# Kernel tuning notes

Measured on AMD Instinct MI355X. Metric: run time of the kernel, lower is better.

## Reference

```python
import jax, jax.numpy as jnp
import numpy as np

# SOM hyperparameters (match init_kwargs)
M, N = 64, 64
NODES = M * N
FEATS = 256
BATCH = 1024
LR = 0.5
RADIUS_FACTOR = 1.1
TOTAL_ITER = 100000
SIGMA = max(M, N) * RADIUS_FACTOR


def setup_inputs() -> dict:
    key = jax.random.key(0)
    k1, k2 = jax.random.split(key)
    x = jax.random.uniform(k1, (BATCH, FEATS), dtype=jnp.float32)
    map_w = jax.random.uniform(k2, (NODES, FEATS), dtype=jnp.float32)
    return {"x": x, "map_w": map_w, "iteration": 0}


def _grid_locs():
    ii, jj = jnp.meshgrid(jnp.arange(M), jnp.arange(N), indexing='ij')
    return jnp.stack([ii.ravel(), jj.ravel()], axis=1)  # (NODES, 2) int32


def reference(x, map_w, iteration):
    B = x.shape[0]
    # ---- feedforward: squared distances (B, NODES) via GEMM expansion,
    # avoiding the (B, NODES, FEATS) broadcast the TF code materializes.
    x2 = jnp.sum(x * x, axis=1, keepdims=True)          # (B, 1)
    w2 = jnp.sum(map_w * map_w, axis=1)                  # (NODES,)
    sqd = x2 + w2[None, :] - 2.0 * (x @ map_w.T)         # (B, NODES)
    bmu_indices = jnp.argmin(sqd, axis=1)                # (B,)

    # ---- backprop: neighborhood-weighted codebook update
    locs = _grid_locs()                                  # (NODES, 2)
    bmu_locs = locs[bmu_indices]                         # (B, 2)
    # grid distance^2 between every node and each sample's BMU: (B, NODES)
    d2 = jnp.sum((locs[None, :, :] - bmu_locs[:, None, :]) ** 2, axis=2).astype(jnp.float32)

    lambda_g = TOTAL_ITER / SIGMA
    decay = jnp.exp(jnp.float32(-float(iteration) / lambda_g))
    radius = SIGMA * decay + 1e-6
    lr = LR * decay

    impact = jnp.exp(-d2 / (2.0 * radius * radius))
    in_radius = (jnp.sqrt(d2) <= radius).astype(jnp.float32)
    lr_op = impact * in_radius * lr                      # (B, NODES)

    # weight_update[n,d] = sum_b lr_op[b,n] * (x[b,d] - map_w[n,d])
    # computed without the (B, NODES, FEATS) intermediate:
    upd = (jnp.einsum('bn,bd->nd', lr_op, x) - lr_op.sum(axis=0)[:, None] * map_w) / B
    new_map = map_w + upd
    return new_map, bmu_indices
```

## Files before the change

### kernel.cpp

```cpp
#include <hip/hip_runtime.h>
#include <math.h>

#define NODES 4096
#define FEATS 256
#define BATCH 1024
#define LR_C 0.5f
#define SIGMA_C 70.4f

typedef _Float16 f16x8 __attribute__((ext_vector_type(8)));
typedef float floatx4 __attribute__((ext_vector_type(4)));

__device__ __forceinline__ void get_params(int it, float& lr, float& r2, float& i2r2) {
    float decay = __expf(-(float)it * (SIGMA_C / 100000.0f));
    float radius = SIGMA_C * decay + 1e-6f;
    lr = LR_C * decay;
    r2 = radius * radius;
    i2r2 = 1.0f / (2.0f * r2);
}

__device__ __forceinline__ unsigned fkey(float f) {
    unsigned u = __float_as_uint(f);
    return (u & 0x80000000u) ? ~u : (u | 0x80000000u);
}
__device__ __forceinline__ unsigned long long shfl_xor_u64(unsigned long long v, int mask) {
    unsigned lo = (unsigned)v, hi = (unsigned)(v >> 32);
    lo = __shfl_xor(lo, mask, 64);
    hi = __shfl_xor(hi, mask, 64);
    return ((unsigned long long)hi << 32) | lo;
}

__global__ __launch_bounds__(256) void k_gemm1min(const float* __restrict__ X, const float* __restrict__ Wm,
                                                  _Float16* __restrict__ XT,
                                                  unsigned long long* __restrict__ gmin) {
    __shared__ _Float16 Ah[64][40];
    __shared__ _Float16 Al[64][40];
    __shared__ _Float16 Bh[64][40];
    __shared__ _Float16 Bl[64][40];
    __shared__ unsigned long long rowmin[64][2];
    __shared__ float w2s[64][4];
    const int n0 = blockIdx.x * 64;
    const int b0 = blockIdx.y * 64;
    const int t = threadIdx.x;
    const int wave = t >> 6, lane = t & 63;
    const int wm = wave & 1, wn = wave >> 1;
    const int lm = lane & 15, quad = lane >> 4;
    const int srow = t >> 2, skoff = (t & 3) * 8;
    float wsq = 0.0f;
    floatx4 acc[2][2] = {};
    for (int k0 = 0; k0 < FEATS; k0 += 32) {
        float xa[8], wa[8];
        *(float4*)&xa[0] = *(const float4*)&X[(size_t)(b0 + srow) * FEATS + k0 + skoff];
        *(float4*)&xa[4] = *(const float4*)&X[(size_t)(b0 + srow) * FEATS + k0 + skoff + 4];
        *(float4*)&wa[0] = *(const float4*)&Wm[(size_t)(n0 + srow) * FEATS + k0 + skoff];
        *(float4*)&wa[4] = *(const float4*)&Wm[(size_t)(n0 + srow) * FEATS + k0 + skoff + 4];
        union { _Float16 h[8]; float4 q; } xh, xl, wh, wl;
#pragma unroll
        for (int i = 0; i < 8; ++i) {
            xh.h[i] = (_Float16)xa[i];
            xl.h[i] = (_Float16)(xa[i] - (float)xh.h[i]);
            wh.h[i] = (_Float16)wa[i];
            wl.h[i] = (_Float16)(wa[i] - (float)wh.h[i]);
            wsq += wa[i] * wa[i];
        }
        *(float4*)&Ah[srow][skoff] = xh.q;
        *(float4*)&Al[srow][skoff] = xl.q;
        *(float4*)&Bh[srow][skoff] = wh.q;
        *(float4*)&Bl[srow][skoff] = wl.q;
        __syncthreads();
        f16x8 ah[2], al[2], bh[2], bl[2];
        ah[0] = *(f16x8*)&Ah[wm * 32 + lm][quad * 8];
        ah[1] = *(f16x8*)&Ah[wm * 32 + 16 + lm][quad * 8];
        al[0] = *(f16x8*)&Al[wm * 32 + lm][quad * 8];
        al[1] = *(f16x8*)&Al[wm * 32 + 16 + lm][quad * 8];
        bh[0] = *(f16x8*)&Bh[wn * 32 + lm][quad * 8];
        bh[1] = *(f16x8*)&Bh[wn * 32 + 16 + lm][quad * 8];
        bl[0] = *(f16x8*)&Bl[wn * 32 + lm][quad * 8];
        bl[1] = *(f16x8*)&Bl[wn * 32 + 16 + lm][quad * 8];
#pragma unroll
        for (int i = 0; i < 2; ++i)
#pragma unroll
            for (int j = 0; j < 2; ++j) {
                acc[i][j] = __builtin_amdgcn_mfma_f32_16x16x32_f16(ah[i], bh[j], acc[i][j], 0, 0, 0);
                acc[i][j] = __builtin_amdgcn_mfma_f32_16x16x32_f16(ah[i], bl[j], acc[i][j], 0, 0, 0);
                acc[i][j] = __builtin_amdgcn_mfma_f32_16x16x32_f16(al[i], bh[j], acc[i][j], 0, 0, 0);
            }
        if (blockIdx.x == (k0 >> 5)) {
            const int dcol = t >> 3, bch = (t & 7) * 8;
            union { _Float16 h[8]; float4 q; } u;
#pragma unroll
            for (int j = 0; j < 8; ++j) u.h[j] = Ah[bch + j][dcol];
            *(float4*)&XT[(size_t)(k0 + dcol) * BATCH + b0 + bch] = u.q;
        }
        __syncthreads();
    }
    w2s[srow][t & 3] = wsq;
    __syncthreads();
    const int col0 = n0 + wn * 32 + lm, col1 = col0 + 16;
    const int r0 = wn * 32 + lm, r1 = r0 + 16;
    const float w20 = w2s[r0][0] + w2s[r0][1] + w2s[r0][2] + w2s[r0][3];
    const float w21 = w2s[r1][0] + w2s[r1][1] + w2s[r1][2] + w2s[r1][3];
#pragma unroll
    for (int i = 0; i < 2; ++i) {
#pragma unroll
        for (int r = 0; r < 4; ++r) {
            float va = w20 - 2.0f * acc[i][0][r];
            float vb = w21 - 2.0f * acc[i][1][r];
            unsigned long long ka = ((unsigned long long)fkey(va) << 32) | (unsigned)col0;
            unsigned long long kb = ((unsigned long long)fkey(vb) << 32) | (unsigned)col1;
            unsigned long long m = ka < kb ? ka : kb;
#pragma unroll
            for (int mk = 1; mk < 16; mk <<= 1) {
                unsigned long long o = shfl_xor_u64(m, mk);
                if (o < m) m = o;
            }
            if (lm == 0) rowmin[wm * 32 + i * 16 + quad * 4 + r][wn] = m;
        }
    }
    __syncthreads();
    if (t < 64) {
        unsigned long long v = rowmin[t][0];
        if (rowmin[t][1] < v) v = rowmin[t][1];
        atomicMin(&gmin[b0 + t], v);
    }
}

__global__ __launch_bounds__(256) void k_gemm2f(const _Float16* __restrict__ XT,
                                                const unsigned long long* __restrict__ gmin,
                                                const int* __restrict__ itp,
                                                const float* __restrict__ Wm,
                                                float* __restrict__ out0, float* __restrict__ out1) {
    __shared__ _Float16 As[32][136];
    __shared__ _Float16 Bs[64][136];
    __shared__ int bmu_s[1024];
    __shared__ float Svl[32];
    const int d0 = blockIdx.x * 64;
    const int n0 = blockIdx.y * 32;
    const int t = threadIdx.x;
    const int wave = t >> 6, lane = t & 63;
    const int wm = wave & 1, wn = wave >> 1;
    const int lm = lane & 15, quad = lane >> 4;

#pragma unroll
    for (int j = 0; j < 4; ++j)
        bmu_s[t + j * 256] = (int)(gmin[t + j * 256] & 0xFFFFFFFFULL);
    float lr, r2, i2r2;
    get_params(itp[0], lr, r2, i2r2);
    if (blockIdx.x == 0 && blockIdx.y < 4)
        out1[blockIdx.y * 256 + t] = (float)(int)(gmin[blockIdx.y * 256 + t] & 0xFFFFFFFFULL);
    __syncthreads();

    const int arow = t >> 3, ac = (t & 7) * 16;
    const int nn = n0 + arow;
    const int ni = nn >> 6, nj = nn & 63;
    const int brow = t >> 2, bcoff = (t & 3) * 32;

    float ssum = 0.0f;
    floatx4 acc0 = {}, acc1 = {};
    for (int k0 = 0; k0 < BATCH; k0 += 128) {
        union { _Float16 h[16]; float4 q[2]; } u;
#pragma unroll
        for (int c = 0; c < 16; ++c) {
            int m = bmu_s[k0 + ac + c];
            int di = ni - (m >> 6); di = di < 0 ? -di : di;
            int dj = nj - (m & 63); dj = dj < 0 ? -dj : dj;
            float d2f = (float)(di * di + dj * dj);
            float val = (d2f <= r2) ? lr * __expf(-d2f * i2r2) : 0.0f;
            u.h[c] = (_Float16)val;
            ssum += val;
        }
        *(float4*)&As[arow][ac] = u.q[0];
        *(float4*)&As[arow][ac + 8] = u.q[1];
#pragma unroll
        for (int c = 0; c < 4; ++c)
            *(float4*)&Bs[brow][bcoff + c * 8] =
                *(const float4*)&XT[(size_t)(d0 + brow) * BATCH + k0 + bcoff + c * 8];
        __syncthreads();
#pragma unroll
        for (int ks = 0; ks < 128; ks += 32) {
            f16x8 a = *(f16x8*)&As[wm * 16 + lm][ks + quad * 8];
            f16x8 b0 = *(f16x8*)&Bs[wn * 32 + lm][ks + quad * 8];
            f16x8 b1 = *(f16x8*)&Bs[wn * 32 + 16 + lm][ks + quad * 8];
            acc0 = __builtin_amdgcn_mfma_f32_16x16x32_f16(a, b0, acc0, 0, 0, 0);
            acc1 = __builtin_amdgcn_mfma_f32_16x16x32_f16(a, b1, acc1, 0, 0, 0);
        }
        __syncthreads();
    }
#pragma unroll
    for (int mk = 1; mk < 8; mk <<= 1) ssum += __shfl_xor(ssum, mk, 64);
    if ((t & 7) == 0) Svl[arow] = ssum;
    __syncthreads();

    const float invB = 1.0f / (float)BATCH;
#pragma unroll
    for (int r = 0; r < 4; ++r) {
        int rowN = n0 + wm * 16 + quad * 4 + r;
        float cc = 1.0f - Svl[rowN - n0] * invB;
        int col0 = d0 + wn * 32 + lm;
        int col1 = col0 + 16;
        out0[(size_t)rowN * FEATS + col0] = Wm[(size_t)rowN * FEATS + col0] * cc + acc0[r] * invB;
        out0[(size_t)rowN * FEATS + col1] = Wm[(size_t)rowN * FEATS + col1] * cc + acc1[r] * invB;
    }
}

extern "C" void kernel_launch(void* const* d_in, const int* in_sizes, int n_in,
                              void* d_out, int out_size, void* d_ws, size_t ws_size,
                              hipStream_t stream) {
    const float* X = (const float*)d_in[0];
    const float* Wm = (const float*)d_in[1];
    const int* itp = (const int*)d_in[2];
    float* out0 = (float*)d_out;
    float* out1 = out0 + (size_t)NODES * FEATS;

    char* ws = (char*)d_ws;
    _Float16* XT = (_Float16*)(ws + 0);
    unsigned long long* gmin = (unsigned long long*)(ws + 524288);

    hipMemsetAsync(gmin, 0xFF, 1024 * sizeof(unsigned long long), stream);
    k_gemm1min<<<dim3(64, 16), 256, 0, stream>>>(X, Wm, XT, gmin);
    k_gemm2f<<<dim3(4, 128), 256, 0, stream>>>(XT, gmin, itp, Wm, out0, out1);
}
```

Measured before the change: 89.81 us.

## Enlarge GEMM1 block tile to 64x128 nodes with K-step 64

The distance GEMM kernel now covers 128 nodes per block instead of 64 and loads 64 features per iteration instead of 32. Each wave computes a 32x64 sub-tile with 8 accumulators. The goal is to reuse each X tile across more nodes, cut the number of barriers, and halve the grid to 512 blocks. The costs are higher register and LDS use and fewer blocks to spread across the CUs. The XT transpose write and the row-min reduction are adjusted to match the new tile.

```diff
diff --git a/kernel.cpp b/kernel.cpp
--- a/kernel.cpp
+++ b/kernel.cpp
@@ -32,88 +32,112 @@
 __global__ __launch_bounds__(256) void k_gemm1min(const float* __restrict__ X, const float* __restrict__ Wm,
                                                   _Float16* __restrict__ XT,
                                                   unsigned long long* __restrict__ gmin) {
-    __shared__ _Float16 Ah[64][40];
-    __shared__ _Float16 Al[64][40];
-    __shared__ _Float16 Bh[64][40];
-    __shared__ _Float16 Bl[64][40];
+    __shared__ _Float16 Ah[64][72];
+    __shared__ _Float16 Al[64][72];
+    __shared__ _Float16 Bh[128][72];
+    __shared__ _Float16 Bl[128][72];
     __shared__ unsigned long long rowmin[64][2];
-    __shared__ float w2s[64][4];
-    const int n0 = blockIdx.x * 64;
+    __shared__ float w2s[128][2];
+    const int n0 = blockIdx.x * 128;
     const int b0 = blockIdx.y * 64;
     const int t = threadIdx.x;
     const int wave = t >> 6, lane = t & 63;
-    const int wm = wave & 1, wn = wave >> 1;
+    const int wb = wave & 1, wn2 = wave >> 1;
     const int lm = lane & 15, quad = lane >> 4;
-    const int srow = t >> 2, skoff = (t & 3) * 8;
+    const int xrow = t >> 2, xk = (t & 3) * 16;
+    const int wrow = t >> 1, wk = (t & 1) * 32;
     float wsq = 0.0f;
-    floatx4 acc[2][2] = {};
-    for (int k0 = 0; k0 < FEATS; k0 += 32) {
-        float xa[8], wa[8];
-        *(float4*)&xa[0] = *(const float4*)&X[(size_t)(b0 + srow) * FEATS + k0 + skoff];
-        *(float4*)&xa[4] = *(const float4*)&X[(size_t)(b0 + srow) * FEATS + k0 + skoff + 4];
-        *(float4*)&wa[0] = *(const float4*)&Wm[(size_t)(n0 + srow) * FEATS + k0 + skoff];
-        *(float4*)&wa[4] = *(const float4*)&Wm[(size_t)(n0 + srow) * FEATS + k0 + skoff + 4];
-        union { _Float16 h[8]; float4 q; } xh, xl, wh, wl;
-#pragma unroll
-        for (int i = 0; i < 8; ++i) {
-            xh.h[i] = (_Float16)xa[i];
-            xl.h[i] = (_Float16)(xa[i] - (float)xh.h[i]);
-            wh.h[i] = (_Float16)wa[i];
-            wl.h[i] = (_Float16)(wa[i] - (float)wh.h[i]);
-            wsq += wa[i] * wa[i];
-        }
-        *(float4*)&Ah[srow][skoff] = xh.q;
-        *(float4*)&Al[srow][skoff] = xl.q;
-        *(float4*)&Bh[srow][skoff] = wh.q;
-        *(float4*)&Bl[srow][skoff] = wl.q;
-        __syncthreads();
-        f16x8 ah[2], al[2], bh[2], bl[2];
-        ah[0] = *(f16x8*)&Ah[wm * 32 + lm][quad * 8];
-        ah[1] = *(f16x8*)&Ah[wm * 32 + 16 + lm][quad * 8];
-        al[0] = *(f16x8*)&Al[wm * 32 + lm][quad * 8];
-        al[1] = *(f16x8*)&Al[wm * 32 + 16 + lm][quad * 8];
-        bh[0] = *(f16x8*)&Bh[wn * 32 + lm][quad * 8];
-        bh[1] = *(f16x8*)&Bh[wn * 32 + 16 + lm][quad * 8];
-        bl[0] = *(f16x8*)&Bl[wn * 32 + lm][quad * 8];
-        bl[1] = *(f16x8*)&Bl[wn * 32 + 16 + lm][quad * 8];
-#pragma unroll
-        for (int i = 0; i < 2; ++i)
-#pragma unroll
-            for (int j = 0; j < 2; ++j) {
-                acc[i][j] = __builtin_amdgcn_mfma_f32_16x16x32_f16(ah[i], bh[j], acc[i][j], 0, 0, 0);
-                acc[i][j] = __builtin_amdgcn_mfma_f32_16x16x32_f16(ah[i], bl[j], acc[i][j], 0, 0, 0);
-                acc[i][j] = __builtin_amdgcn_mfma_f32_16x16x32_f16(al[i], bh[j], acc[i][j], 0, 0, 0);
-            }
-        if (blockIdx.x == (k0 >> 5)) {
-            const int dcol = t >> 3, bch = (t & 7) * 8;
-            union { _Float16 h[8]; float4 q; } u;
-#pragma unroll
-            for (int j = 0; j < 8; ++j) u.h[j] = Ah[bch + j][dcol];
-            *(float4*)&XT[(size_t)(k0 + dcol) * BATCH + b0 + bch] = u.q;
-        }
-        __syncthreads();
-    }
-    w2s[srow][t & 3] = wsq;
-    __syncthreads();
-    const int col0 = n0 + wn * 32 + lm, col1 = col0 + 16;
-    const int r0 = wn * 32 + lm, r1 = r0 + 16;
-    const float w20 = w2s[r0][0] + w2s[r0][1] + w2s[r0][2] + w2s[r0][3];
-    const float w21 = w2s[r1][0] + w2s[r1][1] + w2s[r1][2] + w2s[r1][3];
-#pragma unroll
-    for (int i = 0; i < 2; ++i) {
+    floatx4 acc[2][4] = {};
+    for (int k0 = 0; k0 < FEATS; k0 += 64) {
+#pragma unroll
+        for (int ch = 0; ch < 2; ++ch) {
+            float a[8];
+            *(float4*)&a[0] = *(const float4*)&X[(size_t)(b0 + xrow) * FEATS + k0 + xk + ch * 8];
+            *(float4*)&a[4] = *(const float4*)&X[(size_t)(b0 + xrow) * FEATS + k0 + xk + ch * 8 + 4];
+            union { _Float16 h[8]; float4 q; } hh, ll;
+#pragma unroll
+            for (int i = 0; i < 8; ++i) {
+                hh.h[i] = (_Float16)a[i];
+                ll.h[i] = (_Float16)(a[i] - (float)hh.h[i]);
+            }
+            *(float4*)&Ah[xrow][xk + ch * 8] = hh.q;
+            *(float4*)&Al[xrow][xk + ch * 8] = ll.q;
+        }
+#pragma unroll
+        for (int ch = 0; ch < 4; ++ch) {
+            float a[8];
+            *(float4*)&a[0] = *(const float4*)&Wm[(size_t)(n0 + wrow) * FEATS + k0 + wk + ch * 8];
+            *(float4*)&a[4] = *(const float4*)&Wm[(size_t)(n0 + wrow) * FEATS + k0 + wk + ch * 8 + 4];
+            union { _Float16 h[8]; float4 q; } hh, ll;
+#pragma unroll
+            for (int i = 0; i < 8; ++i) {
+                hh.h[i] = (_Float16)a[i];
+                ll.h[i] = (_Float16)(a[i] - (float)hh.h[i]);
+                wsq += a[i] * a[i];
+            }
+            *(float4*)&Bh[wrow][wk + ch * 8] = hh.q;
+            *(float4*)&Bl[wrow][wk + ch * 8] = ll.q;
+        }
+        __syncthreads();
+#pragma unroll
+        for (int ks = 0; ks < 64; ks += 32) {
+            f16x8 xh[2], xl[2], wh[4], wl[4];
+#pragma unroll
+            for (int bf = 0; bf < 2; ++bf) {
+                xh[bf] = *(f16x8*)&Ah[wb * 32 + bf * 16 + lm][ks + quad * 8];
+                xl[bf] = *(f16x8*)&Al[wb * 32 + bf * 16 + lm][ks + quad * 8];
+            }
+#pragma unroll
+            for (int nf = 0; nf < 4; ++nf) {
+                wh[nf] = *(f16x8*)&Bh[wn2 * 64 + nf * 16 + lm][ks + quad * 8];
+                wl[nf] = *(f16x8*)&Bl[wn2 * 64 + nf * 16 + lm][ks + quad * 8];
+            }
+#pragma unroll
+            for (int bf = 0; bf < 2; ++bf)
+#pragma unroll
+                for (int nf = 0; nf < 4; ++nf) {
+                    acc[bf][nf] = __builtin_amdgcn_mfma_f32_16x16x32_f16(xh[bf], wh[nf], acc[bf][nf], 0, 0, 0);
+                    acc[bf][nf] = __builtin_amdgcn_mfma_f32_16x16x32_f16(xh[bf], wl[nf], acc[bf][nf], 0, 0, 0);
+                    acc[bf][nf] = __builtin_amdgcn_mfma_f32_16x16x32_f16(xl[bf], wh[nf], acc[bf][nf], 0, 0, 0);
+                }
+        }
+        if (blockIdx.x == (k0 >> 6)) {
+            const int dcol = t >> 2, bch = (t & 3) * 16;
+            union { _Float16 h[16]; float4 q[2]; } u;
+#pragma unroll
+            for (int j = 0; j < 16; ++j) u.h[j] = Ah[bch + j][dcol];
+            *(float4*)&XT[(size_t)(k0 + dcol) * BATCH + b0 + bch] = u.q[0];
+            *(float4*)&XT[(size_t)(k0 + dcol) * BATCH + b0 + bch + 8] = u.q[1];
+        }
+        __syncthreads();
+    }
+    w2s[wrow][t & 1] = wsq;
+    __syncthreads();
+    int colg[4];
+    float w2c[4];
+#pragma unroll
+    for (int nf = 0; nf < 4; ++nf) {
+        int rt = wn2 * 64 + nf * 16 + lm;
+        colg[nf] = n0 + rt;
+        w2c[nf] = w2s[rt][0] + w2s[rt][1];
+    }
+#pragma unroll
+    for (int bf = 0; bf < 2; ++bf) {
 #pragma unroll
         for (int r = 0; r < 4; ++r) {
-            float va = w20 - 2.0f * acc[i][0][r];
-            float vb = w21 - 2.0f * acc[i][1][r];
-            unsigned long long ka = ((unsigned long long)fkey(va) << 32) | (unsigned)col0;
-            unsigned long long kb = ((unsigned long long)fkey(vb) << 32) | (unsigned)col1;
-            unsigned long long m = ka < kb ? ka : kb;
+            unsigned long long m = 0xFFFFFFFFFFFFFFFFULL;
+#pragma unroll
+            for (int nf = 0; nf < 4; ++nf) {
+                float v = w2c[nf] - 2.0f * acc[bf][nf][r];
+                unsigned long long k = ((unsigned long long)fkey(v) << 32) | (unsigned)colg[nf];
+                if (k < m) m = k;
+            }
 #pragma unroll
             for (int mk = 1; mk < 16; mk <<= 1) {
                 unsigned long long o = shfl_xor_u64(m, mk);
                 if (o < m) m = o;
             }
-            if (lm == 0) rowmin[wm * 32 + i * 16 + quad * 4 + r][wn] = m;
+            if (lm == 0) rowmin[wb * 32 + bf * 16 + quad * 4 + r][wn2] = m;
         }
     }
     __syncthreads();
@@ -216,6 +240,6 @@
     unsigned long long* gmin = (unsigned long long*)(ws + 524288);
 
     hipMemsetAsync(gmin, 0xFF, 1024 * sizeof(unsigned long long), stream);
-    k_gemm1min<<<dim3(64, 16), 256, 0, stream>>>(X, Wm, XT, gmin);
+    k_gemm1min<<<dim3(32, 16), 256, 0, stream>>>(X, Wm, XT, gmin);
     k_gemm2f<<<dim3(4, 128), 256, 0, stream>>>(XT, gmin, itp, Wm, out0, out1);
 }
```

Result: slower. 92.23 us (+2.7%).
